# Kernel tuning notes

Hardware: AMD Instinct MI355X
Metric: run time of the kernel (lower is better)

Reference implementation:

```python
import jax, jax.numpy as jnp
import numpy as np

N_NODES = 50000
N_GRAPHS = 512
NEG_SLOPE = 0.2
EPS = 1e-16


def gat_conv(x, src, dst, W, a_src, a_dst, b):
    """PyG GATConv (heads=1, self-loops already appended, eval mode)."""
    h = x @ W                                   # [N, out]
    as_ = h @ a_src                             # [N]
    ad_ = h @ a_dst                             # [N]
    e = jax.nn.leaky_relu(as_[src] + ad_[dst], NEG_SLOPE)  # [E]
    # segment softmax over destination node
    m = jax.ops.segment_max(e, dst, num_segments=N_NODES)
    ee = jnp.exp(e - m[dst])
    s = jax.ops.segment_sum(ee, dst, num_segments=N_NODES)
    alpha = ee / (s[dst] + EPS)                 # [E]
    out = jax.ops.segment_sum(h[src] * alpha[:, None], dst, num_segments=N_NODES)
    return out + b


def setup_inputs() -> dict:
    key = jax.random.key(0)
    ks = jax.random.split(key, 16)
    vocab, d_model, hidden = 32000, 128, 128
    node_ids = jax.random.randint(ks[0], (N_NODES,), 0, vocab)
    edge_index = jax.random.randint(ks[1], (2, 800000), 0, N_NODES)
    batch = jnp.sort(jax.random.randint(ks[2], (N_NODES,), 0, N_GRAPHS))
    emb = jax.random.normal(ks[3], (vocab, d_model), jnp.float32) * 0.02

    def layer(k, din, dout):
        k1, k2, k3 = jax.random.split(k, 3)
        W = jax.random.normal(k1, (din, dout), jnp.float32) / np.sqrt(din)
        a_s = jax.random.normal(k2, (dout,), jnp.float32) / np.sqrt(dout)
        a_d = jax.random.normal(k3, (dout,), jnp.float32) / np.sqrt(dout)
        b = jnp.zeros((dout,), jnp.float32)
        return W, a_s, a_d, b

    W1, as1, ad1, b1 = layer(ks[4], d_model, hidden)
    W2, as2, ad2, b2 = layer(ks[5], hidden, hidden)
    W3, as3, ad3, b3 = layer(ks[6], hidden, hidden)
    return dict(node_ids=node_ids, edge_index=edge_index, batch=batch, emb=emb,
                W1=W1, as1=as1, ad1=ad1, b1=b1,
                W2=W2, as2=as2, ad2=ad2, b2=b2,
                W3=W3, as3=as3, ad3=ad3, b3=b3)


def reference(node_ids, edge_index, batch, emb,
              W1, as1, ad1, b1, W2, as2, ad2, b2, W3, as3, ad3, b3):
    # add self-loops (PyG GATConv default)
    loop = jnp.arange(N_NODES, dtype=edge_index.dtype)
    src = jnp.concatenate([edge_index[0], loop])
    dst = jnp.concatenate([edge_index[1], loop])

    x = emb[node_ids]                                   # [N, d_model]
    x = jax.nn.relu(gat_conv(x, src, dst, W1, as1, ad1, b1))
    x = jax.nn.relu(gat_conv(x, src, dst, W2, as2, ad2, b2))
    x = gat_conv(x, src, dst, W3, as3, ad3, b3)

    # global mean pool over graphs
    sums = jax.ops.segment_sum(x, batch, num_segments=N_GRAPHS)
    cnts = jax.ops.segment_sum(jnp.ones((N_NODES,), x.dtype), batch, num_segments=N_GRAPHS)
    return sums / jnp.maximum(cnts, 1.0)[:, None]       # [n_graphs, hidden]
```

## Files before the change

kernel.cpp:

```cpp
#include <hip/hip_runtime.h>
#include <hip/hip_fp16.h>
#include <math.h>

#define N_NODES    50000
#define N_EDGES_IN 800000
#define N_EDGES    850000
#define N_GRAPHS   512
#define NEG_SLOPE  0.2f
#define EPS_F      1e-16f

#define NB_COARSE  196
#define NSUB       8
#define NBINS      (NB_COARSE*NSUB)
#define CAP        1024
#define GEMM_BLOCKS 391

typedef _Float16 half8 __attribute__((ext_vector_type(8)));
typedef float    f32x4 __attribute__((ext_vector_type(4)));

__global__ __launch_bounds__(256) void k_gemm(const void* __restrict__ xsrc,
                                              const int* __restrict__ ids,
                                              const float* __restrict__ W,
                                              const float* __restrict__ a_s,
                                              const float* __restrict__ a_d,
                                              _Float16* __restrict__ hH,
                                              float* __restrict__ as_,
                                              float* __restrict__ ad_) {
    __shared__ _Float16 WT[128][136];
    __shared__ _Float16 Xs[128][72];
    int t = threadIdx.x;
    int row0 = blockIdx.x * 128;
    int w = t >> 6, lane = t & 63;
    int n = lane & 15, quad = lane >> 4;

    #pragma unroll
    for (int i = 0; i < 16; i++) {
        int q = t + i * 256;
        int k = q >> 5;
        int n4 = (q & 31) * 4;
        float4 v = *(const float4*)(W + (size_t)k * 128 + n4);
        WT[n4 + 0][k] = (_Float16)v.x;
        WT[n4 + 1][k] = (_Float16)v.y;
        WT[n4 + 2][k] = (_Float16)v.z;
        WT[n4 + 3][k] = (_Float16)v.w;
    }

    f32x4 acc[2][8] = {};
    for (int kc = 0; kc < 2; kc++) {
        if (kc) __syncthreads();
        if (ids == nullptr) {
            const _Float16* xH = (const _Float16*)xsrc;
            #pragma unroll
            for (int i = 0; i < 4; i++) {
                int q = t + i * 256;
                int r = q >> 3, o8 = (q & 7) * 8;
                int gr = row0 + r; if (gr >= N_NODES) gr = N_NODES - 1;
                *(half8*)&Xs[r][o8] = *(const half8*)&xH[(size_t)gr * 128 + kc * 64 + o8];
            }
        } else {
            const float* xf = (const float*)xsrc;
            #pragma unroll
            for (int i = 0; i < 4; i++) {
                int q = t + i * 256;
                int r = q >> 3, o8 = (q & 7) * 8;
                int gr = row0 + r; if (gr >= N_NODES) gr = N_NODES - 1;
                const float* src = xf + (size_t)ids[gr] * 128 + kc * 64 + o8;
                float4 v0 = *(const float4*)src;
                float4 v1 = *(const float4*)(src + 4);
                half8 hv;
                hv[0] = (_Float16)v0.x; hv[1] = (_Float16)v0.y;
                hv[2] = (_Float16)v0.z; hv[3] = (_Float16)v0.w;
                hv[4] = (_Float16)v1.x; hv[5] = (_Float16)v1.y;
                hv[6] = (_Float16)v1.z; hv[7] = (_Float16)v1.w;
                *(half8*)&Xs[r][o8] = hv;
            }
        }
        __syncthreads();
        #pragma unroll
        for (int ks = 0; ks < 2; ks++) {
            int ko = ks * 32 + quad * 8;
            half8 a0 = *(const half8*)&Xs[w * 32 + n][ko];
            half8 a1 = *(const half8*)&Xs[w * 32 + 16 + n][ko];
            int kg = kc * 64 + ko;
            #pragma unroll
            for (int c = 0; c < 8; c++) {
                half8 b = *(const half8*)&WT[c * 16 + n][kg];
                acc[0][c] = __builtin_amdgcn_mfma_f32_16x16x32_f16(a0, b, acc[0][c], 0, 0, 0);
                acc[1][c] = __builtin_amdgcn_mfma_f32_16x16x32_f16(a1, b, acc[1][c], 0, 0, 0);
            }
        }
    }

    float sa[8], da[8];
    #pragma unroll
    for (int c = 0; c < 8; c++) { sa[c] = a_s[c * 16 + n]; da[c] = a_d[c * 16 + n]; }
    #pragma unroll
    for (int r = 0; r < 2; r++) {
        float ps[4] = {0.f, 0.f, 0.f, 0.f}, pd[4] = {0.f, 0.f, 0.f, 0.f};
        #pragma unroll
        for (int reg = 0; reg < 4; reg++) {
            int row = row0 + w * 32 + r * 16 + quad * 4 + reg;
            bool ok = row < N_NODES;
            #pragma unroll
            for (int c = 0; c < 8; c++) {
                float v = acc[r][c][reg];
                ps[reg] += v * sa[c];
                pd[reg] += v * da[c];
                if (ok) hH[(size_t)row * 128 + c * 16 + n] = (_Float16)v;
            }
        }
        #pragma unroll
        for (int off = 1; off < 16; off <<= 1) {
            #pragma unroll
            for (int reg = 0; reg < 4; reg++) {
                ps[reg] += __shfl_xor(ps[reg], off, 64);
                pd[reg] += __shfl_xor(pd[reg], off, 64);
            }
        }
        if (n == 0) {
            #pragma unroll
            for (int reg = 0; reg < 4; reg++) {
                int row = row0 + w * 32 + r * 16 + quad * 4 + reg;
                if (row < N_NODES) { as_[row] = ps[reg]; ad_[row] = pd[reg]; }
            }
        }
    }
}

__global__ __launch_bounds__(256) void k_scat1(const int* __restrict__ ei,
                                               int* __restrict__ gcur,
                                               int* __restrict__ recs) {
    __shared__ int lcnt[NB_COARSE];
    __shared__ int lbase[NB_COARSE];
    int t = threadIdx.x;
    int e0 = blockIdx.x * 4096;
    int sub = blockIdx.x & 7;
    for (int i = t; i < NB_COARSE; i += 256) lcnt[i] = 0;
    __syncthreads();
    int rec[16], b[16], r[16];
    #pragma unroll
    for (int i = 0; i < 16; i++) {
        int e = e0 + t + i * 256;
        if (e < N_EDGES) {
            int s, d;
            if (e < N_EDGES_IN) { s = ei[e]; d = ei[N_EDGES_IN + e]; }
            else                { s = e - N_EDGES_IN; d = s; }
            b[i] = d >> 8;
            rec[i] = s | ((d & 255) << 16);
            r[i] = atomicAdd(&lcnt[b[i]], 1);
        } else b[i] = -1;
    }
    __syncthreads();
    for (int i = t; i < NB_COARSE; i += 256) {
        int c = lcnt[i];
        lbase[i] = c ? atomicAdd(&gcur[i * NSUB + sub], c) : 0;
    }
    __syncthreads();
    #pragma unroll
    for (int i = 0; i < 16; i++)
        if (b[i] >= 0) recs[(b[i] * NSUB + sub) * CAP + lbase[b[i]] + r[i]] = rec[i];
}

__global__ __launch_bounds__(256) void k_scat2(const int* __restrict__ recs,
                                               const int* __restrict__ gcur,
                                               int* __restrict__ row_ptr,
                                               int* __restrict__ srcs) {
    __shared__ int scnt[NBINS];
    __shared__ int bcnt[256];
    __shared__ int hist[256];
    __shared__ int off2[256];
    __shared__ int rank[256];
    int b = blockIdx.x, t = threadIdx.x;
    for (int i = t; i < NBINS; i += 256) scnt[i] = gcur[i];
    hist[t] = 0; rank[t] = 0;
    __syncthreads();
    int tot = 0;
    if (t < NB_COARSE) {
        #pragma unroll
        for (int s = 0; s < NSUB; s++) tot += scnt[t * NSUB + s];
    }
    bcnt[t] = tot;
    __syncthreads();
    for (int o = 1; o < 256; o <<= 1) {
        int x = (t >= o) ? bcnt[t - o] : 0;
        __syncthreads(); bcnt[t] += x; __syncthreads();
    }
    int lo = (b == 0) ? 0 : bcnt[b - 1];
    for (int s = 0; s < NSUB; s++) {
        int c = scnt[b * NSUB + s];
        const int* reg = &recs[(b * NSUB + s) * CAP];
        for (int i = t; i < c; i += 256) atomicAdd(&hist[reg[i] >> 16], 1);
    }
    __syncthreads();
    int v = hist[t];
    off2[t] = v; __syncthreads();
    for (int o = 1; o < 256; o <<= 1) {
        int x = (t >= o) ? off2[t - o] : 0;
        __syncthreads(); off2[t] += x; __syncthreads();
    }
    int excl = off2[t] - v;
    int dglob = b * 256 + t;
    if (dglob < N_NODES) row_ptr[dglob] = lo + excl;
    if (b == 0 && t == 0) row_ptr[N_NODES] = N_EDGES;
    __syncthreads();
    off2[t] = excl;
    __syncthreads();
    for (int s = 0; s < NSUB; s++) {
        int c = scnt[b * NSUB + s];
        const int* reg = &recs[(b * NSUB + s) * CAP];
        for (int i = t; i < c; i += 256) {
            int rec = reg[i];
            int dl = rec >> 16;
            int rk = atomicAdd(&rank[dl], 1);
            srcs[lo + off2[dl] + rk] = rec & 0xFFFF;
        }
    }
}

__global__ __launch_bounds__(256) void k_aggregate(
        const float4* __restrict__ h16,
        const float* __restrict__ as_,
        const float* __restrict__ ad_, const int* __restrict__ row_ptr,
        const int* __restrict__ srcs, const float4* __restrict__ bias4,
        float4* __restrict__ xout16, int do_relu) {
    int d = (blockIdx.x * blockDim.x + threadIdx.x) >> 4;
    if (d >= N_NODES) return;
    int lane = threadIdx.x & 63;
    int gl   = lane & 15;
    int base = lane & 48;
    int lo = row_ptr[d], hi = row_ptr[d + 1];
    int deg = hi - lo;
    float add = ad_[d];

    float eC[4]; int sC[4];
    float m_l = -1e30f, s_l = 0.f;
    #pragma unroll
    for (int c = 0; c < 4; c++) {
        float e = -1e30f; int sidx = 0;
        int j = c * 16 + gl;
        if (j < deg) {
            sidx = __builtin_nontemporal_load(&srcs[lo + j]);
            e = as_[sidx] + add;
            e = (e > 0.f) ? e : NEG_SLOPE * e;
            float nm = fmaxf(m_l, e);
            s_l = s_l * __expf(m_l - nm) + __expf(e - nm);
            m_l = nm;
        }
        eC[c] = e; sC[c] = sidx;
    }
    for (int j0 = 64; j0 < deg; j0 += 16) {
        int j = j0 + gl;
        if (j < deg) {
            int sidx = __builtin_nontemporal_load(&srcs[lo + j]);
            float e = as_[sidx] + add;
            e = (e > 0.f) ? e : NEG_SLOPE * e;
            float nm = fmaxf(m_l, e);
            s_l = s_l * __expf(m_l - nm) + __expf(e - nm);
            m_l = nm;
        }
    }
    float m = m_l, s = s_l;
    #pragma unroll
    for (int off = 8; off; off >>= 1) {
        float om = __shfl_xor(m, off, 64);
        float os = __shfl_xor(s, off, 64);
        float nm = fmaxf(m, om);
        s = s * __expf(m - nm) + os * __expf(om - nm);
        m = nm;
    }
    float inv = 1.f / (s + EPS_F);

    float4 acc0 = make_float4(0.f, 0.f, 0.f, 0.f);
    float4 acc1 = make_float4(0.f, 0.f, 0.f, 0.f);
    #pragma unroll
    for (int c = 0; c < 4; c++) {
        int j0 = c * 16;
        if (j0 >= deg) break;
        float w = __expf(eC[c] - m) * inv;
        int sidx = sC[c];
        int cnt = min(16, deg - j0);
        for (int jj = 0; jj < cnt; jj += 4) {
            float w0 = __shfl(w, base + jj + 0, 64); int s0 = __shfl(sidx, base + jj + 0, 64);
            float w1 = __shfl(w, base + jj + 1, 64); int s1 = __shfl(sidx, base + jj + 1, 64);
            float w2 = __shfl(w, base + jj + 2, 64); int s2 = __shfl(sidx, base + jj + 2, 64);
            float w3 = __shfl(w, base + jj + 3, 64); int s3 = __shfl(sidx, base + jj + 3, 64);
            float4 r0 = h16[(size_t)s0 * 16 + gl];
            float4 r1 = h16[(size_t)s1 * 16 + gl];
            float4 r2 = h16[(size_t)s2 * 16 + gl];
            float4 r3 = h16[(size_t)s3 * 16 + gl];
            const __half2* p;
            float2 f0, f1, f2, f3;
            p = (const __half2*)&r0;
            f0 = __half22float2(p[0]); f1 = __half22float2(p[1]);
            f2 = __half22float2(p[2]); f3 = __half22float2(p[3]);
            acc0.x += w0*f0.x; acc0.y += w0*f0.y; acc0.z += w0*f1.x; acc0.w += w0*f1.y;
            acc1.x += w0*f2.x; acc1.y += w0*f2.y; acc1.z += w0*f3.x; acc1.w += w0*f3.y;
            p = (const __half2*)&r1;
            f0 = __half22float2(p[0]); f1 = __half22float2(p[1]);
            f2 = __half22float2(p[2]); f3 = __half22float2(p[3]);
            acc0.x += w1*f0.x; acc0.y += w1*f0.y; acc0.z += w1*f1.x; acc0.w += w1*f1.y;
            acc1.x += w1*f2.x; acc1.y += w1*f2.y; acc1.z += w1*f3.x; acc1.w += w1*f3.y;
            p = (const __half2*)&r2;
            f0 = __half22float2(p[0]); f1 = __half22float2(p[1]);
            f2 = __half22float2(p[2]); f3 = __half22float2(p[3]);
            acc0.x += w2*f0.x; acc0.y += w2*f0.y; acc0.z += w2*f1.x; acc0.w += w2*f1.y;
            acc1.x += w2*f2.x; acc1.y += w2*f2.y; acc1.z += w2*f3.x; acc1.w += w2*f3.y;
            p = (const __half2*)&r3;
            f0 = __half22float2(p[0]); f1 = __half22float2(p[1]);
            f2 = __half22float2(p[2]); f3 = __half22float2(p[3]);
            acc0.x += w3*f0.x; acc0.y += w3*f0.y; acc0.z += w3*f1.x; acc0.w += w3*f1.y;
            acc1.x += w3*f2.x; acc1.y += w3*f2.y; acc1.z += w3*f3.x; acc1.w += w3*f3.y;
        }
    }
    for (int j0 = 64; j0 < deg; j0 += 16) {
        int j = j0 + gl;
        float w = 0.f; int sidx = 0;
        if (j < deg) {
            int si = __builtin_nontemporal_load(&srcs[lo + j]);
            float e = as_[si] + add;
            e = (e > 0.f) ? e : NEG_SLOPE * e;
            w = __expf(e - m) * inv;
            sidx = si;
        }
        int cnt = min(16, deg - j0);
        for (int jj = 0; jj < cnt; jj++) {
            float w0 = __shfl(w, base + jj, 64); int s0 = __shfl(sidx, base + jj, 64);
            float4 r0 = h16[(size_t)s0 * 16 + gl];
            const __half2* p = (const __half2*)&r0;
            float2 f0 = __half22float2(p[0]), f1 = __half22float2(p[1]);
            float2 f2 = __half22float2(p[2]), f3 = __half22float2(p[3]);
            acc0.x += w0*f0.x; acc0.y += w0*f0.y; acc0.z += w0*f1.x; acc0.w += w0*f1.y;
            acc1.x += w0*f2.x; acc1.y += w0*f2.y; acc1.z += w0*f3.x; acc1.w += w0*f3.y;
        }
    }
    float4 b0 = bias4[gl * 2], b1 = bias4[gl * 2 + 1];
    float4 o0 = make_float4(acc0.x + b0.x, acc0.y + b0.y, acc0.z + b0.z, acc0.w + b0.w);
    float4 o1 = make_float4(acc1.x + b1.x, acc1.y + b1.y, acc1.z + b1.z, acc1.w + b1.w);
    if (do_relu) {
        o0.x = fmaxf(o0.x, 0.f); o0.y = fmaxf(o0.y, 0.f);
        o0.z = fmaxf(o0.z, 0.f); o0.w = fmaxf(o0.w, 0.f);
        o1.x = fmaxf(o1.x, 0.f); o1.y = fmaxf(o1.y, 0.f);
        o1.z = fmaxf(o1.z, 0.f); o1.w = fmaxf(o1.w, 0.f);
    }
    union { __half2 h2[4]; float4 f; } pk;
    pk.h2[0] = __floats2half2_rn(o0.x, o0.y);
    pk.h2[1] = __floats2half2_rn(o0.z, o0.w);
    pk.h2[2] = __floats2half2_rn(o1.x, o1.y);
    pk.h2[3] = __floats2half2_rn(o1.z, o1.w);
    xout16[(size_t)d * 16 + gl] = pk.f;
}

__global__ __launch_bounds__(512) void k_pool(const __half* __restrict__ x,
                                              const int* __restrict__ batch,
                                              float* __restrict__ out) {
    __shared__ float red[512];
    __shared__ int sh[2];
    int g = blockIdx.x;
    int t = threadIdx.x;
    if (t == 0) {
        int lo = 0, hi = N_NODES;
        while (lo < hi) { int mid = (lo + hi) >> 1; if (batch[mid] < g) lo = mid + 1; else hi = mid; }
        sh[0] = lo;
        int lo2 = lo, hi2 = N_NODES;
        while (lo2 < hi2) { int mid = (lo2 + hi2) >> 1; if (batch[mid] < g + 1) lo2 = mid + 1; else hi2 = mid; }
        sh[1] = lo2;
    }
    __syncthreads();
    int lo = sh[0], hi = sh[1];
    int sub = t >> 7, dim = t & 127;
    float sum = 0.f;
    for (int i = lo + sub; i < hi; i += 4) sum += __half2float(x[(size_t)i * 128 + dim]);
    red[t] = sum;
    __syncthreads();
    if (t < 128) {
        float s = red[t] + red[t + 128] + red[t + 256] + red[t + 384];
        int cnt = hi - lo;
        out[g * 128 + t] = s * (cnt > 0 ? 1.f / (float)cnt : 1.f);
    }
}

extern "C" void kernel_launch(void* const* d_in, const int* in_sizes, int n_in,
                              void* d_out, int out_size, void* d_ws, size_t ws_size,
                              hipStream_t stream) {
    const int*   node_ids   = (const int*)d_in[0];
    const int*   edge_index = (const int*)d_in[1];
    const int*   batch      = (const int*)d_in[2];
    const float* emb        = (const float*)d_in[3];
    const float* W[3]  = {(const float*)d_in[4],  (const float*)d_in[8],  (const float*)d_in[12]};
    const float* As[3] = {(const float*)d_in[5],  (const float*)d_in[9],  (const float*)d_in[13]};
    const float* Ad[3] = {(const float*)d_in[6],  (const float*)d_in[10], (const float*)d_in[14]};
    const float* Bs[3] = {(const float*)d_in[7],  (const float*)d_in[11], (const float*)d_in[15]};

    char* ws = (char*)d_ws;
    size_t off = 0;
    auto alloc = [&](size_t bytes) {
        void* p = ws + off; off += (bytes + 255) & ~(size_t)255; return p;
    };
    _Float16* xH    = (_Float16*)alloc((size_t)N_NODES * 128 * 2);
    _Float16* hH    = (_Float16*)alloc((size_t)N_NODES * 128 * 2);
    float*  as_     = (float*)alloc((size_t)N_NODES * 4);
    float*  ad_     = (float*)alloc((size_t)N_NODES * 4);
    int*    gcur    = (int*)alloc((size_t)NBINS * 4);
    int*    row_ptr = (int*)alloc((size_t)(N_NODES + 1) * 4);
    int*    recs    = (int*)alloc((size_t)NBINS * CAP * 4);
    int*    srcs    = (int*)alloc((size_t)N_EDGES * 4);
    (void)ws_size; (void)in_sizes; (void)n_in; (void)out_size;

    hipMemsetAsync(gcur, 0, (size_t)NBINS * 4, stream);

    k_scat1<<<(N_EDGES + 4095) / 4096, 256, 0, stream>>>(edge_index, gcur, recs);
    k_scat2<<<NB_COARSE, 256, 0, stream>>>(recs, gcur, row_ptr, srcs);

    for (int l = 0; l < 3; l++) {
        k_gemm<<<GEMM_BLOCKS, 256, 0, stream>>>(
                 (l == 0) ? (const void*)emb : (const void*)xH,
                 (l == 0) ? node_ids : nullptr,
                 W[l], As[l], Ad[l], hH, as_, ad_);
        k_aggregate<<<(N_NODES * 16 + 255) / 256, 256, 0, stream>>>((const float4*)hH,
                 as_, ad_, row_ptr, srcs, (const float4*)Bs[l], (float4*)xH,
                 (l < 2) ? 1 : 0);
    }
    k_pool<<<N_GRAPHS, 512, 0, stream>>>((const __half*)xH, batch, (float*)d_out);
}
```

Before: 292.1 us.

## Fuse first-layer embedding GEMM with CSR scatter pass into one launch

Merges the layer-0 gather-GEMM and the second CSR-building pass into a single kernel whose blocks are split by index: the first GEMM_BLOCKS blocks do the GEMM and the remaining blocks do the scatter. The two are independent, so they can run concurrently on the GPU instead of back to back, and one launch is removed. Shared memory becomes a manually partitioned 53 KB buffer sized for the larger role, which can reduce occupancy for the scatter blocks.

Result: faster. 284.4 us, median of 3 (-2.6%).

```diff
diff --git a/kernel.cpp b/kernel.cpp
--- a/kernel.cpp
+++ b/kernel.cpp
@@ -18,18 +18,21 @@
 typedef _Float16 half8 __attribute__((ext_vector_type(8)));
 typedef float    f32x4 __attribute__((ext_vector_type(4)));
 
-__global__ __launch_bounds__(256) void k_gemm(const void* __restrict__ xsrc,
-                                              const int* __restrict__ ids,
-                                              const float* __restrict__ W,
-                                              const float* __restrict__ a_s,
-                                              const float* __restrict__ a_d,
-                                              _Float16* __restrict__ hH,
-                                              float* __restrict__ as_,
-                                              float* __restrict__ ad_) {
-    __shared__ _Float16 WT[128][136];
-    __shared__ _Float16 Xs[128][72];
+template<bool GATHER>
+__device__ __forceinline__ void gemm_body(
+        _Float16 (* __restrict__ WT)[136],
+        _Float16 (* __restrict__ Xs)[72],
+        const void* __restrict__ xsrc,
+        const int* __restrict__ ids,
+        const float* __restrict__ W,
+        const float* __restrict__ a_s,
+        const float* __restrict__ a_d,
+        _Float16* __restrict__ hH,
+        float* __restrict__ as_,
+        float* __restrict__ ad_,
+        int blk) {
     int t = threadIdx.x;
-    int row0 = blockIdx.x * 128;
+    int row0 = blk * 128;
     int w = t >> 6, lane = t & 63;
     int n = lane & 15, quad = lane >> 4;
 
@@ -48,7 +51,7 @@
     f32x4 acc[2][8] = {};
     for (int kc = 0; kc < 2; kc++) {
         if (kc) __syncthreads();
-        if (ids == nullptr) {
+        if (!GATHER) {
             const _Float16* xH = (const _Float16*)xsrc;
             #pragma unroll
             for (int i = 0; i < 4; i++) {
@@ -127,6 +130,105 @@
     }
 }
 
+__device__ __forceinline__ void scat2_body(
+        int* __restrict__ scnt,
+        int* __restrict__ bcnt,
+        int* __restrict__ hist,
+        int* __restrict__ off2,
+        int* __restrict__ rank,
+        const int* __restrict__ recs,
+        const int* __restrict__ gcur,
+        int* __restrict__ row_ptr,
+        int* __restrict__ srcs,
+        int b) {
+    int t = threadIdx.x;
+    for (int i = t; i < NBINS; i += 256) scnt[i] = gcur[i];
+    hist[t] = 0; rank[t] = 0;
+    __syncthreads();
+    int tot = 0;
+    if (t < NB_COARSE) {
+        #pragma unroll
+        for (int s = 0; s < NSUB; s++) tot += scnt[t * NSUB + s];
+    }
+    bcnt[t] = tot;
+    __syncthreads();
+    for (int o = 1; o < 256; o <<= 1) {
+        int x = (t >= o) ? bcnt[t - o] : 0;
+        __syncthreads(); bcnt[t] += x; __syncthreads();
+    }
+    int lo = (b == 0) ? 0 : bcnt[b - 1];
+    for (int s = 0; s < NSUB; s++) {
+        int c = scnt[b * NSUB + s];
+        const int* reg = &recs[(b * NSUB + s) * CAP];
+        for (int i = t; i < c; i += 256) atomicAdd(&hist[reg[i] >> 16], 1);
+    }
+    __syncthreads();
+    int v = hist[t];
+    off2[t] = v; __syncthreads();
+    for (int o = 1; o < 256; o <<= 1) {
+        int x = (t >= o) ? off2[t - o] : 0;
+        __syncthreads(); off2[t] += x; __syncthreads();
+    }
+    int excl = off2[t] - v;
+    int dglob = b * 256 + t;
+    if (dglob < N_NODES) row_ptr[dglob] = lo + excl;
+    if (b == 0 && t == 0) row_ptr[N_NODES] = N_EDGES;
+    __syncthreads();
+    off2[t] = excl;
+    __syncthreads();
+    for (int s = 0; s < NSUB; s++) {
+        int c = scnt[b * NSUB + s];
+        const int* reg = &recs[(b * NSUB + s) * CAP];
+        for (int i = t; i < c; i += 256) {
+            int rec = reg[i];
+            int dl = rec >> 16;
+            int rk = atomicAdd(&rank[dl], 1);
+            srcs[lo + off2[dl] + rk] = rec & 0xFFFF;
+        }
+    }
+}
+
+__global__ __launch_bounds__(256) void k_gemm(const void* __restrict__ xsrc,
+                                              const float* __restrict__ W,
+                                              const float* __restrict__ a_s,
+                                              const float* __restrict__ a_d,
+                                              _Float16* __restrict__ hH,
+                                              float* __restrict__ as_,
+                                              float* __restrict__ ad_) {
+    __shared__ _Float16 WT[128][136];
+    __shared__ _Float16 Xs[128][72];
+    gemm_body<false>(WT, Xs, xsrc, nullptr, W, a_s, a_d, hH, as_, ad_, blockIdx.x);
+}
+
+__global__ __launch_bounds__(256) void k_gemm0_scat2(
+        const float* __restrict__ emb,
+        const int* __restrict__ ids,
+        const float* __restrict__ W,
+        const float* __restrict__ a_s,
+        const float* __restrict__ a_d,
+        _Float16* __restrict__ hH,
+        float* __restrict__ as_,
+        float* __restrict__ ad_,
+        const int* __restrict__ recs,
+        const int* __restrict__ gcur,
+        int* __restrict__ row_ptr,
+        int* __restrict__ srcs) {
+    __shared__ __align__(16) char smem[53248];
+    if (blockIdx.x < GEMM_BLOCKS) {
+        _Float16 (*WT)[136] = (_Float16(*)[136])smem;
+        _Float16 (*Xs)[72]  = (_Float16(*)[72])(smem + 34816);
+        gemm_body<true>(WT, Xs, emb, ids, W, a_s, a_d, hH, as_, ad_, blockIdx.x);
+    } else {
+        int* scnt = (int*)smem;
+        int* bcnt = scnt + NBINS;
+        int* hist = bcnt + 256;
+        int* off2 = hist + 256;
+        int* rank = off2 + 256;
+        scat2_body(scnt, bcnt, hist, off2, rank, recs, gcur, row_ptr, srcs,
+                   blockIdx.x - GEMM_BLOCKS);
+    }
+}
+
 __global__ __launch_bounds__(256) void k_scat1(const int* __restrict__ ei,
                                                int* __restrict__ gcur,
                                                int* __restrict__ recs) {
@@ -159,62 +261,6 @@
     #pragma unroll
     for (int i = 0; i < 16; i++)
         if (b[i] >= 0) recs[(b[i] * NSUB + sub) * CAP + lbase[b[i]] + r[i]] = rec[i];
-}
-
-__global__ __launch_bounds__(256) void k_scat2(const int* __restrict__ recs,
-                                               const int* __restrict__ gcur,
-                                               int* __restrict__ row_ptr,
-                                               int* __restrict__ srcs) {
-    __shared__ int scnt[NBINS];
-    __shared__ int bcnt[256];
-    __shared__ int hist[256];
-    __shared__ int off2[256];
-    __shared__ int rank[256];
-    int b = blockIdx.x, t = threadIdx.x;
-    for (int i = t; i < NBINS; i += 256) scnt[i] = gcur[i];
-    hist[t] = 0; rank[t] = 0;
-    __syncthreads();
-    int tot = 0;
-    if (t < NB_COARSE) {
-        #pragma unroll
-        for (int s = 0; s < NSUB; s++) tot += scnt[t * NSUB + s];
-    }
-    bcnt[t] = tot;
-    __syncthreads();
-    for (int o = 1; o < 256; o <<= 1) {
-        int x = (t >= o) ? bcnt[t - o] : 0;
-        __syncthreads(); bcnt[t] += x; __syncthreads();
-    }
-    int lo = (b == 0) ? 0 : bcnt[b - 1];
-    for (int s = 0; s < NSUB; s++) {
-        int c = scnt[b * NSUB + s];
-        const int* reg = &recs[(b * NSUB + s) * CAP];
-        for (int i = t; i < c; i += 256) atomicAdd(&hist[reg[i] >> 16], 1);
-    }
-    __syncthreads();
-    int v = hist[t];
-    off2[t] = v; __syncthreads();
-    for (int o = 1; o < 256; o <<= 1) {
-        int x = (t >= o) ? off2[t - o] : 0;
-        __syncthreads(); off2[t] += x; __syncthreads();
-    }
-    int excl = off2[t] - v;
-    int dglob = b * 256 + t;
-    if (dglob < N_NODES) row_ptr[dglob] = lo + excl;
-    if (b == 0 && t == 0) row_ptr[N_NODES] = N_EDGES;
-    __syncthreads();
-    off2[t] = excl;
-    __syncthreads();
-    for (int s = 0; s < NSUB; s++) {
-        int c = scnt[b * NSUB + s];
-        const int* reg = &recs[(b * NSUB + s) * CAP];
-        for (int i = t; i < c; i += 256) {
-            int rec = reg[i];
-            int dl = rec >> 16;
-            int rk = atomicAdd(&rank[dl], 1);
-            srcs[lo + off2[dl] + rk] = rec & 0xFFFF;
-        }
-    }
 }
 
 __global__ __launch_bounds__(256) void k_aggregate(
@@ -409,13 +455,15 @@
     hipMemsetAsync(gcur, 0, (size_t)NBINS * 4, stream);
 
     k_scat1<<<(N_EDGES + 4095) / 4096, 256, 0, stream>>>(edge_index, gcur, recs);
-    k_scat2<<<NB_COARSE, 256, 0, stream>>>(recs, gcur, row_ptr, srcs);
+
+    k_gemm0_scat2<<<GEMM_BLOCKS + NB_COARSE, 256, 0, stream>>>(
+            emb, node_ids, W[0], As[0], Ad[0], hH, as_, ad_,
+            recs, gcur, row_ptr, srcs);
 
     for (int l = 0; l < 3; l++) {
-        k_gemm<<<GEMM_BLOCKS, 256, 0, stream>>>(
-                 (l == 0) ? (const void*)emb : (const void*)xH,
-                 (l == 0) ? node_ids : nullptr,
-                 W[l], As[l], Ad[l], hH, as_, ad_);
+        if (l > 0)
+            k_gemm<<<GEMM_BLOCKS, 256, 0, stream>>>(
+                     (const void*)xH, W[l], As[l], Ad[l], hH, as_, ad_);
         k_aggregate<<<(N_NODES * 16 + 255) / 256, 256, 0, stream>>>((const float4*)hH,
                  as_, ad_, row_ptr, srcs, (const float4*)Bs[l], (float4*)xH,
                  (l < 2) ? 1 : 0);
```
